# Kernel tuning notes

Measured on AMD Instinct MI355X. Metric: run time of the kernel, lower is better.

The kernel has to match this reference:

```python
import jax, jax.numpy as jnp
import numpy as np

HIDDEN = 256
HEADS = 8
HEAD_DIM = HIDDEN // HEADS
N = 4096
EPS = 1e-5


def setup_inputs() -> dict:
    key = jax.random.key(0)
    ks = jax.random.split(key, 16)
    s = HIDDEN ** -0.5
    inp = {
        "A": jax.random.uniform(ks[0], (N, N), dtype=jnp.float32),
        "h": jax.random.normal(ks[1], (N, HIDDEN), dtype=jnp.float32),
        # Linear layers stored torch-style as [out, in]
        "Wq": jax.random.normal(ks[2], (HIDDEN, HIDDEN), jnp.float32) * s,
        "bq": jnp.zeros((HIDDEN,), jnp.float32),
        "Wk": jax.random.normal(ks[3], (HIDDEN, HIDDEN), jnp.float32) * s,
        "bk": jnp.zeros((HIDDEN,), jnp.float32),
        "Wv": jax.random.normal(ks[4], (HIDDEN, HIDDEN), jnp.float32) * s,
        "bv": jnp.zeros((HIDDEN,), jnp.float32),
        "Wo": jax.random.normal(ks[5], (HIDDEN, HIDDEN), jnp.float32) * s,
        "bo": jnp.zeros((HIDDEN,), jnp.float32),
        "W1": jax.random.normal(ks[6], (2 * HIDDEN, HIDDEN), jnp.float32) * s,
        "c1": jnp.zeros((2 * HIDDEN,), jnp.float32),
        "W2": jax.random.normal(ks[7], (HIDDEN, 2 * HIDDEN), jnp.float32) * (2 * HIDDEN) ** -0.5,
        "c2": jnp.zeros((HIDDEN,), jnp.float32),
        "g1": jnp.ones((HIDDEN,), jnp.float32),
        "be1": jnp.zeros((HIDDEN,), jnp.float32),
        "g2": jnp.ones((HIDDEN,), jnp.float32),
        "be2": jnp.zeros((HIDDEN,), jnp.float32),
    }
    return inp


def _batchnorm(x, gamma, beta):
    # BatchNorm1d training mode: biased batch stats over node axis
    mean = x.mean(axis=0)
    var = ((x - mean) ** 2).mean(axis=0)
    return (x - mean) * jax.lax.rsqrt(var + EPS) * gamma + beta


def _mha(A, h, Wq, bq, Wk, bk, Wv, bv, Wo, bo):
    n = h.shape[0]
    scaling = HEAD_DIM ** -0.5
    # NOTE: raw reshape [N, H*d] -> (H, N, d), exactly as the torch code (no transpose)
    q = ((h @ Wq.T + bq).reshape(HEADS, n, HEAD_DIM)) * scaling
    k = (h @ Wk.T + bk).reshape(HEADS, n, HEAD_DIM)
    v = (h @ Wv.T + bv).reshape(HEADS, n, HEAD_DIM)
    t = jnp.einsum('hnd,hmd->hnm', q, k)          # [H, N, N]
    attn = jax.nn.softmax(t * A, axis=2)          # multiplicative adjacency mask
    out = jnp.einsum('hnm,hmd->hnd', attn, v)     # [H, N, d]
    return out.reshape(n, -1) @ Wo.T + bo         # raw reshape back, as in torch


def reference(A, h, Wq, bq, Wk, bk, Wv, bv, Wo, bo, W1, c1, W2, c2, g1, be1, g2, be2):
    h1 = h
    x = _mha(A, h, Wq, bq, Wk, bk, Wv, bv, Wo, bo)
    x = _batchnorm(x + h1, g1, be1)
    h2 = x
    x = jax.nn.relu(x @ W1.T + c1) @ W2.T + c2
    return _batchnorm(h2 + x, g2, be2)
```

## Files before the change

kernel.cpp:

```cpp
#include <hip/hip_runtime.h>

#define N_NODES 4096
#define HID 256
#define NHEADS 8
#define HDIM 32
#define EPSV 1e-5f
#define M2LOG 11.541560327111707f

typedef __bf16 bf16x8 __attribute__((ext_vector_type(8)));
typedef __bf16 bf16x4 __attribute__((ext_vector_type(4)));
typedef float f32x4 __attribute__((ext_vector_type(4)));

__device__ inline float fexp2(float x) {
    float r;
    asm("v_exp_f32 %0, %1" : "=v"(r) : "v"(x));
    return r;
}

__device__ inline uint4 pack8(float4 a, float4 b) {
    bf16x8 p;
    p[0]=(__bf16)a.x; p[1]=(__bf16)a.y; p[2]=(__bf16)a.z; p[3]=(__bf16)a.w;
    p[4]=(__bf16)b.x; p[5]=(__bf16)b.y; p[6]=(__bf16)b.z; p[7]=(__bf16)b.w;
    return __builtin_bit_cast(uint4, p);
}
__device__ inline float4 nmad4(float4 x, float4 s, float4 sh) {
    return make_float4(fmaf(x.x,s.x,sh.x), fmaf(x.y,s.y,sh.y),
                       fmaf(x.z,s.z,sh.z), fmaf(x.w,s.w,sh.w));
}

__launch_bounds__(256)
__global__ void gemm_mfma(const float* __restrict__ X, const float* __restrict__ W,
                          const float* __restrict__ bias, const float* __restrict__ resid,
                          float* __restrict__ C,
                          const float* __restrict__ nscale, const float* __restrict__ nshift,
                          const float* __restrict__ rscale, const float* __restrict__ rshift,
                          float* __restrict__ psum, float* __restrict__ pq,
                          int M, int N, int K, float scale, int do_relu) {
    __shared__ uint4 xl[2][512];
    __shared__ uint4 wl[2][512];
    const int bm = blockIdx.x * 64, bn = blockIdx.y * 64;
    const int t = threadIdx.x;
    const int w = t >> 6, l = t & 63, g = l >> 4, nl = l & 15;
    const int srow = t >> 3, seg = t & 7;
    const int sx = (seg & 3) << 1;
    const int d0 = seg*64 + (srow ^ sx);
    const int d1 = seg*64 + ((srow + 32) ^ sx);
    const float* xp = X + (size_t)(bm + srow)*K + seg*8;
    const float* wp = W + (size_t)(bn + srow)*K + seg*8;
    const size_t rstep = (size_t)32*K;

    f32x4 acc[4];
    #pragma unroll
    for (int nf = 0; nf < 4; ++nf) acc[nf] = (f32x4){0.f,0.f,0.f,0.f};

    {
        float4 x0 = *(const float4*)(xp),          x1 = *(const float4*)(xp + 4);
        float4 x2 = *(const float4*)(xp + rstep),  x3 = *(const float4*)(xp + rstep + 4);
        if (nscale) {
            float4 s0 = *(const float4*)(nscale + seg*8), s1 = *(const float4*)(nscale + seg*8 + 4);
            float4 h0 = *(const float4*)(nshift + seg*8), h1 = *(const float4*)(nshift + seg*8 + 4);
            x0 = nmad4(x0,s0,h0); x1 = nmad4(x1,s1,h1);
            x2 = nmad4(x2,s0,h0); x3 = nmad4(x3,s1,h1);
        }
        float4 w0 = *(const float4*)(wp),          w1 = *(const float4*)(wp + 4);
        float4 w2 = *(const float4*)(wp + rstep),  w3 = *(const float4*)(wp + rstep + 4);
        xl[0][d0] = pack8(x0, x1); xl[0][d1] = pack8(x2, x3);
        wl[0][d0] = pack8(w0, w1); wl[0][d1] = pack8(w2, w3);
    }
    __syncthreads();

    for (int k0 = 0; k0 < K; k0 += 64) {
        const int cur = (k0 >> 6) & 1;
        const bool nxt = (k0 + 64) < K;
        float4 nx0, nx1, nx2, nx3, nw0, nw1, nw2, nw3;
        if (nxt) {
            const int kk = k0 + 64;
            nx0 = *(const float4*)(xp + kk);          nx1 = *(const float4*)(xp + kk + 4);
            nx2 = *(const float4*)(xp + rstep + kk);  nx3 = *(const float4*)(xp + rstep + kk + 4);
            if (nscale) {
                float4 s0 = *(const float4*)(nscale + kk + seg*8), s1 = *(const float4*)(nscale + kk + seg*8 + 4);
                float4 h0 = *(const float4*)(nshift + kk + seg*8), h1 = *(const float4*)(nshift + kk + seg*8 + 4);
                nx0 = nmad4(nx0,s0,h0); nx1 = nmad4(nx1,s1,h1);
                nx2 = nmad4(nx2,s0,h0); nx3 = nmad4(nx3,s1,h1);
            }
            nw0 = *(const float4*)(wp + kk);          nw1 = *(const float4*)(wp + kk + 4);
            nw2 = *(const float4*)(wp + rstep + kk);  nw3 = *(const float4*)(wp + rstep + kk + 4);
        }
        __builtin_amdgcn_s_setprio(1);
        #pragma unroll
        for (int ks = 0; ks < 2; ++ks) {
            bf16x8 af = __builtin_bit_cast(bf16x8, xl[cur][(ks*4 + g)*64 + ((w*16 + nl) ^ (g << 1))]);
            #pragma unroll
            for (int nf = 0; nf < 4; ++nf) {
                bf16x8 bfr = __builtin_bit_cast(bf16x8, wl[cur][(ks*4 + g)*64 + ((nf*16 + nl) ^ (g << 1))]);
                acc[nf] = __builtin_amdgcn_mfma_f32_16x16x32_bf16(af, bfr, acc[nf], 0, 0, 0);
            }
        }
        __builtin_amdgcn_s_setprio(0);
        if (nxt) {
            xl[cur^1][d0] = pack8(nx0, nx1); xl[cur^1][d1] = pack8(nx2, nx3);
            wl[cur^1][d0] = pack8(nw0, nw1); wl[cur^1][d1] = pack8(nw2, nw3);
        }
        __syncthreads();
    }

    float colS[4] = {0.f,0.f,0.f,0.f}, colQ[4] = {0.f,0.f,0.f,0.f};
    #pragma unroll
    for (int nf = 0; nf < 4; ++nf) {
        const int col = bn + nf*16 + nl;
        const float bb = bias[col];
        float rs = 1.f, rh = 0.f;
        if (rscale) { rs = rscale[col]; rh = rshift[col]; }
        #pragma unroll
        for (int r = 0; r < 4; ++r) {
            const int row = bm + w*16 + g*4 + r;
            float v = acc[nf][r] + bb;
            if (resid) {
                float rv = resid[(size_t)row*N + col];
                v += rscale ? fmaf(rv, rs, rh) : rv;
            }
            v *= scale;
            if (do_relu) v = fmaxf(v, 0.f);
            C[(size_t)row*N + col] = v;
            colS[nf] += v;
            colQ[nf] = fmaf(v, v, colQ[nf]);
        }
    }
    if (psum) {
        float* cs = (float*)&xl[0][0];
        float* cq = cs + 1024;
        #pragma unroll
        for (int nf = 0; nf < 4; ++nf) {
            const int idx = (w*4 + g)*64 + nf*16 + nl;
            cs[idx] = colS[nf];
            cq[idx] = colQ[nf];
        }
        __syncthreads();
        if (t < 64) {
            float s = 0.f, q = 0.f;
            #pragma unroll
            for (int i = 0; i < 16; ++i) { s += cs[i*64 + t]; q += cq[i*64 + t]; }
            psum[blockIdx.x*HID + bn + t] = s;
            pq[blockIdx.x*HID + bn + t]   = q;
        }
    }
}

__launch_bounds__(256)
__global__ void gemm_wo(const float* __restrict__ Opart, const float* __restrict__ Lpart,
                        int nsplit, const float* __restrict__ W,
                        const float* __restrict__ bias, const float* __restrict__ resid,
                        float* __restrict__ C, float* __restrict__ psum, float* __restrict__ pq) {
    const int N = 256, K = 256;
    __shared__ uint4 xl[2][512];
    __shared__ uint4 wl[2][512];
    const int bm = blockIdx.x * 64, bn = blockIdx.y * 64;
    const int t = threadIdx.x;
    const int w = t >> 6, l = t & 63, g = l >> 4, nl = l & 15;
    const int srow = t >> 3, seg = t & 7;
    const int sx = (seg & 3) << 1;
    const int d0 = seg*64 + (srow ^ sx);
    const int d1 = seg*64 + ((srow + 32) ^ sx);
    const float* wp = W + (size_t)(bn + srow)*K + seg*8;
    const size_t rstep = (size_t)32*K;

    auto cl = [&](int row, int kk, float4& a, float4& b) {
        const size_t flat = (size_t)row*256 + kk;
        const int hn = (int)(flat >> 5);
        float L = 0.f;
        a = make_float4(0.f,0.f,0.f,0.f);
        b = make_float4(0.f,0.f,0.f,0.f);
        for (int z = 0; z < nsplit; ++z) {
            L += Lpart[z*32768 + hn];
            float4 u = *(const float4*)(Opart + (size_t)z*1048576 + flat);
            float4 v = *(const float4*)(Opart + (size_t)z*1048576 + flat + 4);
            a.x += u.x; a.y += u.y; a.z += u.z; a.w += u.w;
            b.x += v.x; b.y += v.y; b.z += v.z; b.w += v.w;
        }
        const float inv = 1.f / L;
        a.x *= inv; a.y *= inv; a.z *= inv; a.w *= inv;
        b.x *= inv; b.y *= inv; b.z *= inv; b.w *= inv;
    };

    f32x4 acc[4];
    #pragma unroll
    for (int nf = 0; nf < 4; ++nf) acc[nf] = (f32x4){0.f,0.f,0.f,0.f};

    {
        float4 x0, x1, x2, x3;
        cl(bm + srow,      seg*8, x0, x1);
        cl(bm + srow + 32, seg*8, x2, x3);
        float4 w0 = *(const float4*)(wp),          w1 = *(const float4*)(wp + 4);
        float4 w2 = *(const float4*)(wp + rstep),  w3 = *(const float4*)(wp + rstep + 4);
        xl[0][d0] = pack8(x0, x1); xl[0][d1] = pack8(x2, x3);
        wl[0][d0] = pack8(w0, w1); wl[0][d1] = pack8(w2, w3);
    }
    __syncthreads();

    for (int k0 = 0; k0 < K; k0 += 64) {
        const int cur = (k0 >> 6) & 1;
        const bool nxt = (k0 + 64) < K;
        float4 nx0, nx1, nx2, nx3, nw0, nw1, nw2, nw3;
        if (nxt) {
            const int kk = k0 + 64 + seg*8;
            cl(bm + srow,      kk, nx0, nx1);
            cl(bm + srow + 32, kk, nx2, nx3);
            nw0 = *(const float4*)(wp + k0 + 64);          nw1 = *(const float4*)(wp + k0 + 68);
            nw2 = *(const float4*)(wp + rstep + k0 + 64);  nw3 = *(const float4*)(wp + rstep + k0 + 68);
        }
        __builtin_amdgcn_s_setprio(1);
        #pragma unroll
        for (int ks = 0; ks < 2; ++ks) {
            bf16x8 af = __builtin_bit_cast(bf16x8, xl[cur][(ks*4 + g)*64 + ((w*16 + nl) ^ (g << 1))]);
            #pragma unroll
            for (int nf = 0; nf < 4; ++nf) {
                bf16x8 bfr = __builtin_bit_cast(bf16x8, wl[cur][(ks*4 + g)*64 + ((nf*16 + nl) ^ (g << 1))]);
                acc[nf] = __builtin_amdgcn_mfma_f32_16x16x32_bf16(af, bfr, acc[nf], 0, 0, 0);
            }
        }
        __builtin_amdgcn_s_setprio(0);
        if (nxt) {
            xl[cur^1][d0] = pack8(nx0, nx1); xl[cur^1][d1] = pack8(nx2, nx3);
            wl[cur^1][d0] = pack8(nw0, nw1); wl[cur^1][d1] = pack8(nw2, nw3);
        }
        __syncthreads();
    }

    float colS[4] = {0.f,0.f,0.f,0.f}, colQ[4] = {0.f,0.f,0.f,0.f};
    #pragma unroll
    for (int nf = 0; nf < 4; ++nf) {
        const int col = bn + nf*16 + nl;
        const float bb = bias[col];
        #pragma unroll
        for (int r = 0; r < 4; ++r) {
            const int row = bm + w*16 + g*4 + r;
            float v = acc[nf][r] + bb + resid[(size_t)row*N + col];
            C[(size_t)row*N + col] = v;
            colS[nf] += v;
            colQ[nf] = fmaf(v, v, colQ[nf]);
        }
    }
    {
        float* cs = (float*)&xl[0][0];
        float* cq = cs + 1024;
        #pragma unroll
        for (int nf = 0; nf < 4; ++nf) {
            const int idx = (w*4 + g)*64 + nf*16 + nl;
            cs[idx] = colS[nf];
            cq[idx] = colQ[nf];
        }
        __syncthreads();
        if (t < 64) {
            float s = 0.f, q = 0.f;
            #pragma unroll
            for (int i = 0; i < 16; ++i) { s += cs[i*64 + t]; q += cq[i*64 + t]; }
            psum[blockIdx.x*HID + bn + t] = s;
            pq[blockIdx.x*HID + bn + t]   = q;
        }
    }
}

__launch_bounds__(256)
__global__ void gemm_qkv(const float* __restrict__ X,
                         const float* __restrict__ Wq, const float* __restrict__ Wk,
                         const float* __restrict__ Wv, const float* __restrict__ bq,
                         const float* __restrict__ bk, const float* __restrict__ bv,
                         __bf16* __restrict__ qhat, __bf16* __restrict__ khat,
                         __bf16* __restrict__ vhat) {
    const int K = 256;
    __shared__ uint4 xl[2][512];
    __shared__ uint4 wl[2][512];
    const int z = blockIdx.z;
    const float* W = (z == 0) ? Wq : (z == 1) ? Wk : Wv;
    const float* bias = (z == 0) ? bq : (z == 1) ? bk : bv;
    __bf16* hat = (z == 0) ? qhat : (z == 1) ? khat : vhat;
    const float scale = (z == 0) ? 0.25506595325f : 1.f;

    const int bm = blockIdx.x * 64, bn = blockIdx.y * 64;
    const int t = threadIdx.x;
    const int w = t >> 6, l = t & 63, g = l >> 4, nl = l & 15;
    const int srow = t >> 3, seg = t & 7;
    const int sx = (seg & 3) << 1;
    const int d0 = seg*64 + (srow ^ sx);
    const int d1 = seg*64 + ((srow + 32) ^ sx);
    const float* xp = X + (size_t)(bm + srow)*K + seg*8;
    const float* wp = W + (size_t)(bn + srow)*K + seg*8;
    const size_t rstep = (size_t)32*K;

    f32x4 acc[4];
    #pragma unroll
    for (int nf = 0; nf < 4; ++nf) acc[nf] = (f32x4){0.f,0.f,0.f,0.f};

    {
        float4 x0 = *(const float4*)(xp),          x1 = *(const float4*)(xp + 4);
        float4 x2 = *(const float4*)(xp + rstep),  x3 = *(const float4*)(xp + rstep + 4);
        float4 w0 = *(const float4*)(wp),          w1 = *(const float4*)(wp + 4);
        float4 w2 = *(const float4*)(wp + rstep),  w3 = *(const float4*)(wp + rstep + 4);
        xl[0][d0] = pack8(x0, x1); xl[0][d1] = pack8(x2, x3);
        wl[0][d0] = pack8(w0, w1); wl[0][d1] = pack8(w2, w3);
    }
    __syncthreads();

    for (int k0 = 0; k0 < K; k0 += 64) {
        const int cur = (k0 >> 6) & 1;
        const bool nxt = (k0 + 64) < K;
        float4 nx0, nx1, nx2, nx3, nw0, nw1, nw2, nw3;
        if (nxt) {
            nx0 = *(const float4*)(xp + k0 + 64);          nx1 = *(const float4*)(xp + k0 + 68);
            nx2 = *(const float4*)(xp + rstep + k0 + 64);  nx3 = *(const float4*)(xp + rstep + k0 + 68);
            nw0 = *(const float4*)(wp + k0 + 64);          nw1 = *(const float4*)(wp + k0 + 68);
            nw2 = *(const float4*)(wp + rstep + k0 + 64);  nw3 = *(const float4*)(wp + rstep + k0 + 68);
        }
        __builtin_amdgcn_s_setprio(1);
        #pragma unroll
        for (int ks = 0; ks < 2; ++ks) {
            bf16x8 af = __builtin_bit_cast(bf16x8, xl[cur][(ks*4 + g)*64 + ((w*16 + nl) ^ (g << 1))]);
            #pragma unroll
            for (int nf = 0; nf < 4; ++nf) {
                bf16x8 bfr = __builtin_bit_cast(bf16x8, wl[cur][(ks*4 + g)*64 + ((nf*16 + nl) ^ (g << 1))]);
                acc[nf] = __builtin_amdgcn_mfma_f32_16x16x32_bf16(af, bfr, acc[nf], 0, 0, 0);
            }
        }
        __builtin_amdgcn_s_setprio(0);
        if (nxt) {
            xl[cur^1][d0] = pack8(nx0, nx1); xl[cur^1][d1] = pack8(nx2, nx3);
            wl[cur^1][d0] = pack8(nw0, nw1); wl[cur^1][d1] = pack8(nw2, nw3);
        }
        __syncthreads();
    }

    #pragma unroll
    for (int nf = 0; nf < 4; ++nf) {
        const int col = bn + nf*16 + nl;
        const float bb = bias[col];
        #pragma unroll
        for (int r = 0; r < 4; ++r) {
            const int row = bm + w*16 + g*4 + r;
            float v = (acc[nf][r] + bb) * scale;
            const int hh = row >> 9;
            const int nn = ((row & 511) << 3) | (col >> 5);
            hat[((size_t)(hh*4096 + nn))*32 + (col & 31)] = (__bf16)v;
        }
    }
}

__launch_bounds__(256)
__global__ void transpose_vhat(const __bf16* __restrict__ vhat, __bf16* __restrict__ vT) {
    const int h = blockIdx.y, n0 = blockIdx.x * 64;
    __shared__ __bf16 tile[64][40];
    const int t = threadIdx.x;
    {
        int n = t >> 2, dd0 = (t & 3) * 8;
        *(uint4*)&tile[n][dd0] = *(const uint4*)(vhat + ((size_t)(h*4096 + n0 + n))*32 + dd0);
    }
    __syncthreads();
    {
        int d = t >> 3, ns = (t & 7) * 8;
        uint4 ov;
        __bf16* op = (__bf16*)&ov;
        #pragma unroll
        for (int j = 0; j < 8; ++j) op[j] = tile[ns + j][d];
        *(uint4*)(vT + ((size_t)(h*32 + d))*4096 + n0 + ns) = ov;
    }
}

__launch_bounds__(512, 2)
__global__ void attn_mfma(const __bf16* __restrict__ qh_, const __bf16* __restrict__ kh,
                          const __bf16* __restrict__ vT, const float* __restrict__ A,
                          float* __restrict__ Opart, float* __restrict__ Lpart, int mlen) {
    __shared__ float A_lds[2][64][68];
    __shared__ uint4 p_lds[8][4][64];

    const int t = threadIdx.x;
    const int w = t >> 6, l = t & 63;
    const int g = l >> 4, nl = l & 15;
    const int n0 = blockIdx.x * 64;
    const int z = blockIdx.y;
    const int m_begin = z * mlen;
    const int nsteps = mlen >> 6;

    bf16x8 qf[4];
    #pragma unroll
    for (int nf = 0; nf < 4; ++nf)
        qf[nf] = *(const bf16x8*)(qh_ + ((size_t)(w*4096 + n0 + nf*16 + nl))*32 + g*8);

    f32x4 oacc[4][2];
    #pragma unroll
    for (int nf = 0; nf < 4; ++nf) {
        oacc[nf][0] = (f32x4){0.f,0.f,0.f,0.f};
        oacc[nf][1] = (f32x4){0.f,0.f,0.f,0.f};
    }
    float Li[4] = {0.f, 0.f, 0.f, 0.f};

    const int aq = t >> 3, am = (t & 7) * 8;
    const float* Abase = A + (size_t)(n0 + aq)*N_NODES + m_begin + am;
    const __bf16* kbase = kh + ((size_t)w*4096 + nl)*32 + g*8;
    const __bf16* vbase = vT + ((size_t)w*32 + nl)*4096 + g*8;

    *(float4*)&A_lds[0][aq][am]   = *(const float4*)(Abase);
    *(float4*)&A_lds[0][aq][am+4] = *(const float4*)(Abase + 4);
    __syncthreads();

    for (int s = 0; s < nsteps; ++s) {
        const int cur = s & 1;
        const int m0 = m_begin + s*64;
        const bool nxt = (s + 1) < nsteps;
        float4 a0n, a1n;
        if (nxt) {
            a0n = *(const float4*)(Abase + (s+1)*64);
            a1n = *(const float4*)(Abase + (s+1)*64 + 4);
        }
        bf16x8 kf[4], vf[4];
        #pragma unroll
        for (int tt = 0; tt < 4; ++tt)
            kf[tt] = *(const bf16x8*)(kbase + (size_t)(m0 + tt*16)*32);
        #pragma unroll
        for (int half = 0; half < 2; ++half)
            #pragma unroll
            for (int dt = 0; dt < 2; ++dt)
                vf[half*2+dt] = *(const bf16x8*)(vbase + (size_t)dt*16*4096 + m0 + half*32);
        __builtin_amdgcn_sched_barrier(0);

        #pragma unroll
        for (int half = 0; half < 2; ++half) {
            #pragma unroll
            for (int tt2 = 0; tt2 < 2; ++tt2) {
                const int tt = half*2 + tt2;
                f32x4 st[4];
                __builtin_amdgcn_s_setprio(1);
                #pragma unroll
                for (int nf = 0; nf < 4; ++nf) {
                    f32x4 zz = (f32x4){0.f,0.f,0.f,0.f};
                    st[nf] = __builtin_amdgcn_mfma_f32_16x16x32_bf16(kf[tt], qf[nf], zz, 0, 0, 0);
                }
                __builtin_amdgcn_s_setprio(0);
                #pragma unroll
                for (int nf = 0; nf < 4; ++nf) {
                    const f32x4 a4 = *(const f32x4*)&A_lds[cur][nf*16 + nl][tt*16 + g*4];
                    float p0 = fexp2(fmaf(st[nf][0], a4[0], -M2LOG));
                    float p1 = fexp2(fmaf(st[nf][1], a4[1], -M2LOG));
                    float p2 = fexp2(fmaf(st[nf][2], a4[2], -M2LOG));
                    float p3 = fexp2(fmaf(st[nf][3], a4[3], -M2LOG));
                    Li[nf] += (p0 + p1) + (p2 + p3);
                    bf16x4 pk;
                    pk[0] = (__bf16)p0; pk[1] = (__bf16)p1;
                    pk[2] = (__bf16)p2; pk[3] = (__bf16)p3;
                    const int gm = tt2*2 + (g >> 1);
                    *(bf16x4*)((char*)&p_lds[w][nf][0] + (gm*16 + (nl ^ (gm << 1)))*16 + (g & 1)*8) = pk;
                }
            }
            __builtin_amdgcn_s_setprio(1);
            #pragma unroll
            for (int nf = 0; nf < 4; ++nf) {
                bf16x8 pf = __builtin_bit_cast(bf16x8, p_lds[w][nf][g*16 + (nl ^ (g << 1))]);
                oacc[nf][0] = __builtin_amdgcn_mfma_f32_16x16x32_bf16(vf[half*2+0], pf, oacc[nf][0], 0, 0, 0);
                oacc[nf][1] = __builtin_amdgcn_mfma_f32_16x16x32_bf16(vf[half*2+1], pf, oacc[nf][1], 0, 0, 0);
            }
            __builtin_amdgcn_s_setprio(0);
        }

        if (nxt) {
            *(float4*)&A_lds[cur^1][aq][am]   = a0n;
            *(float4*)&A_lds[cur^1][aq][am+4] = a1n;
        }
        __syncthreads();
    }

    #pragma unroll
    for (int nf = 0; nf < 4; ++nf) {
        Li[nf] += __shfl_xor(Li[nf], 16);
        Li[nf] += __shfl_xor(Li[nf], 32);
        const int nq = n0 + nf*16 + nl;
        float* ob = Opart + ((size_t)(z*NHEADS + w)*4096 + nq)*32;
        *(float4*)(ob + 0*16 + g*4) = make_float4(oacc[nf][0][0], oacc[nf][0][1],
                                                  oacc[nf][0][2], oacc[nf][0][3]);
        *(float4*)(ob + 1*16 + g*4) = make_float4(oacc[nf][1][0], oacc[nf][1][1],
                                                  oacc[nf][1][2], oacc[nf][1][3]);
        if (g == 0)
            Lpart[(z*NHEADS + w)*4096 + nq] = Li[nf];
    }
}

__launch_bounds__(256)
__global__ void colstats_fin(const float* __restrict__ ps, const float* __restrict__ pq,
                             const float* __restrict__ gam, const float* __restrict__ bet,
                             float* __restrict__ scl, float* __restrict__ shf) {
    const int c = threadIdx.x;
    float s = 0.f, q = 0.f;
    #pragma unroll 8
    for (int b = 0; b < 64; ++b) { s += ps[b*HID + c]; q += pq[b*HID + c]; }
    const float m = s * (1.f/4096.f);
    const float rstd = rsqrtf(q*(1.f/4096.f) - m*m + EPSV);
    const float sc = rstd * gam[c];
    scl[c] = sc;
    shf[c] = fmaf(-m, sc, bet[c]);
}

__launch_bounds__(256)
__global__ void bnorm_apply4(const float* __restrict__ X, const float* __restrict__ scl,
                             const float* __restrict__ shf, float* __restrict__ Y) {
    const int base = (blockIdx.x * 256 + threadIdx.x) * 4;
    const int c = base & (HID - 1);
    float4 x = *(const float4*)(X + base);
    float4 o;
    o.x = fmaf(x.x, scl[c+0], shf[c+0]);
    o.y = fmaf(x.y, scl[c+1], shf[c+1]);
    o.z = fmaf(x.z, scl[c+2], shf[c+2]);
    o.w = fmaf(x.w, scl[c+3], shf[c+3]);
    *(float4*)(Y + base) = o;
}

extern "C" void kernel_launch(void* const* d_in, const int* in_sizes, int n_in,
                              void* d_out, int out_size, void* d_ws, size_t ws_size,
                              hipStream_t stream) {
    const float* A  = (const float*)d_in[0];
    const float* h  = (const float*)d_in[1];
    const float* Wq = (const float*)d_in[2];
    const float* bq = (const float*)d_in[3];
    const float* Wk = (const float*)d_in[4];
    const float* bk = (const float*)d_in[5];
    const float* Wv = (const float*)d_in[6];
    const float* bv = (const float*)d_in[7];
    const float* Wo = (const float*)d_in[8];
    const float* bo = (const float*)d_in[9];
    const float* W1 = (const float*)d_in[10];
    const float* c1 = (const float*)d_in[11];
    const float* W2 = (const float*)d_in[12];
    const float* c2 = (const float*)d_in[13];
    const float* g1 = (const float*)d_in[14];
    const float* be1= (const float*)d_in[15];
    const float* g2 = (const float*)d_in[16];
    const float* be2= (const float*)d_in[17];

    char* wsb = (char*)d_ws;
    const size_t MiB = (size_t)1 << 20;
    const int nsplit = (ws_size >= 43*MiB) ? 8 : (ws_size >= 26*MiB) ? 4 : 2;
    const int mlen = N_NODES / nsplit;

    __bf16* qhat = (__bf16*)(wsb + 0*MiB);
    __bf16* khat = (__bf16*)(wsb + 2*MiB);
    __bf16* vhat = (__bf16*)(wsb + 4*MiB);
    __bf16* vT   = (__bf16*)(wsb + 6*MiB);
    float* Opart = (float*)(wsb + 8*MiB);
    float* Lpart = (float*)(wsb + 8*MiB + (size_t)nsplit*4*MiB);
    char* statb  = wsb + 8*MiB + (size_t)nsplit*4*MiB + 1*MiB;
    float* partS = (float*)statb;
    float* partQ = partS + 64*HID;
    float* scale1 = partQ + 64*HID;
    float* shift1 = scale1 + HID;
    float* scale2 = shift1 + HID;
    float* shift2 = scale2 + HID;
    float* Y1 = (float*)(wsb + 4*MiB);
    float* F1 = (float*)(wsb + 8*MiB);
    float* Y2 = (float*)(wsb + 0*MiB);

    gemm_qkv<<<dim3(64, 4, 3), 256, 0, stream>>>(h, Wq, Wk, Wv, bq, bk, bv, qhat, khat, vhat);
    transpose_vhat<<<dim3(64, 8), 256, 0, stream>>>(vhat, vT);

    attn_mfma<<<dim3(64, nsplit), 512, 0, stream>>>(qhat, khat, vT, A, Opart, Lpart, mlen);

    gemm_wo<<<dim3(64, 4), 256, 0, stream>>>(Opart, Lpart, nsplit, Wo, bo, h, Y1, partS, partQ);
    colstats_fin<<<1, 256, 0, stream>>>(partS, partQ, g1, be1, scale1, shift1);

    gemm_mfma<<<dim3(64, 8), 256, 0, stream>>>(Y1, W1, c1, nullptr, F1,
                                               scale1, shift1, nullptr, nullptr,
                                               nullptr, nullptr, 4096, 512, 256, 1.f, 1);
    gemm_mfma<<<dim3(64, 4), 256, 0, stream>>>(F1, W2, c2, Y1, Y2,
                                               nullptr, nullptr, scale1, shift1,
                                               partS, partQ, 4096, 256, 512, 1.f, 0);
    colstats_fin<<<1, 256, 0, stream>>>(partS, partQ, g2, be2, scale2, shift2);
    bnorm_apply4<<<1024, 256, 0, stream>>>(Y2, scale2, shift2, (float*)d_out);
}
```

Before: 130.2 us.

## Fuse batchnorm stat finalization into consumers and halve attention query tile

The two single-block colstats_fin launches are removed. Each consuming kernel (both FFN GEMMs and a merged finalize-and-apply kernel) now recomputes per-channel scale and shift from the partial sums into shared memory. This drops launches and serialization points at the cost of redundant reduction work per block. Separately, the attention kernel processes 32 query rows per block instead of 64, doubling the grid and raising the occupancy hint to 6 blocks per CU. That gives more parallelism but reuses each K/V fragment across fewer queries.

```diff
diff --git a/kernel.cpp b/kernel.cpp
--- a/kernel.cpp
+++ b/kernel.cpp
@@ -32,12 +32,15 @@
 __global__ void gemm_mfma(const float* __restrict__ X, const float* __restrict__ W,
                           const float* __restrict__ bias, const float* __restrict__ resid,
                           float* __restrict__ C,
-                          const float* __restrict__ nscale, const float* __restrict__ nshift,
-                          const float* __restrict__ rscale, const float* __restrict__ rshift,
+                          const float* __restrict__ pSin, const float* __restrict__ pQin,
+                          const float* __restrict__ gamin, const float* __restrict__ betin,
+                          int norm_x, int norm_r,
                           float* __restrict__ psum, float* __restrict__ pq,
                           int M, int N, int K, float scale, int do_relu) {
     __shared__ uint4 xl[2][512];
     __shared__ uint4 wl[2][512];
+    __shared__ __align__(16) float nsc[256];
+    __shared__ __align__(16) float nsh[256];
     const int bm = blockIdx.x * 64, bn = blockIdx.y * 64;
     const int t = threadIdx.x;
     const int w = t >> 6, l = t & 63, g = l >> 4, nl = l & 15;
@@ -49,6 +52,18 @@
     const float* wp = W + (size_t)(bn + srow)*K + seg*8;
     const size_t rstep = (size_t)32*K;
 
+    if (pSin) {
+        float s = 0.f, q = 0.f;
+        #pragma unroll 8
+        for (int b = 0; b < 64; ++b) { s += pSin[b*HID + t]; q += pQin[b*HID + t]; }
+        const float m = s * (1.f/4096.f);
+        const float rstd = rsqrtf(q*(1.f/4096.f) - m*m + EPSV);
+        const float sc = rstd * gamin[t];
+        nsc[t] = sc;
+        nsh[t] = fmaf(-m, sc, betin[t]);
+        __syncthreads();
+    }
+
     f32x4 acc[4];
     #pragma unroll
     for (int nf = 0; nf < 4; ++nf) acc[nf] = (f32x4){0.f,0.f,0.f,0.f};
@@ -56,9 +71,9 @@
     {
         float4 x0 = *(const float4*)(xp),          x1 = *(const float4*)(xp + 4);
         float4 x2 = *(const float4*)(xp + rstep),  x3 = *(const float4*)(xp + rstep + 4);
-        if (nscale) {
-            float4 s0 = *(const float4*)(nscale + seg*8), s1 = *(const float4*)(nscale + seg*8 + 4);
-            float4 h0 = *(const float4*)(nshift + seg*8), h1 = *(const float4*)(nshift + seg*8 + 4);
+        if (norm_x) {
+            float4 s0 = *(const float4*)(nsc + seg*8), s1 = *(const float4*)(nsc + seg*8 + 4);
+            float4 h0 = *(const float4*)(nsh + seg*8), h1 = *(const float4*)(nsh + seg*8 + 4);
             x0 = nmad4(x0,s0,h0); x1 = nmad4(x1,s1,h1);
             x2 = nmad4(x2,s0,h0); x3 = nmad4(x3,s1,h1);
         }
@@ -77,9 +92,9 @@
             const int kk = k0 + 64;
             nx0 = *(const float4*)(xp + kk);          nx1 = *(const float4*)(xp + kk + 4);
             nx2 = *(const float4*)(xp + rstep + kk);  nx3 = *(const float4*)(xp + rstep + kk + 4);
-            if (nscale) {
-                float4 s0 = *(const float4*)(nscale + kk + seg*8), s1 = *(const float4*)(nscale + kk + seg*8 + 4);
-                float4 h0 = *(const float4*)(nshift + kk + seg*8), h1 = *(const float4*)(nshift + kk + seg*8 + 4);
+            if (norm_x) {
+                float4 s0 = *(const float4*)(nsc + kk + seg*8), s1 = *(const float4*)(nsc + kk + seg*8 + 4);
+                float4 h0 = *(const float4*)(nsh + kk + seg*8), h1 = *(const float4*)(nsh + kk + seg*8 + 4);
                 nx0 = nmad4(nx0,s0,h0); nx1 = nmad4(nx1,s1,h1);
                 nx2 = nmad4(nx2,s0,h0); nx3 = nmad4(nx3,s1,h1);
             }
@@ -110,14 +125,14 @@
         const int col = bn + nf*16 + nl;
         const float bb = bias[col];
         float rs = 1.f, rh = 0.f;
-        if (rscale) { rs = rscale[col]; rh = rshift[col]; }
+        if (norm_r) { rs = nsc[col]; rh = nsh[col]; }
         #pragma unroll
         for (int r = 0; r < 4; ++r) {
             const int row = bm + w*16 + g*4 + r;
             float v = acc[nf][r] + bb;
             if (resid) {
                 float rv = resid[(size_t)row*N + col];
-                v += rscale ? fmaf(rv, rs, rh) : rv;
+                v += norm_r ? fmaf(rv, rs, rh) : rv;
             }
             v *= scale;
             if (do_relu) v = fmaxf(v, 0.f);
@@ -364,52 +379,49 @@
     }
 }
 
-__launch_bounds__(512, 2)
+__launch_bounds__(512, 6)
 __global__ void attn_mfma(const __bf16* __restrict__ qh_, const __bf16* __restrict__ kh,
                           const __bf16* __restrict__ vT, const float* __restrict__ A,
                           float* __restrict__ Opart, float* __restrict__ Lpart, int mlen) {
-    __shared__ float A_lds[2][64][68];
-    __shared__ uint4 p_lds[8][4][64];
+    __shared__ float A_lds[2][32][68];
+    __shared__ uint4 p_lds[8][2][64];
 
     const int t = threadIdx.x;
     const int w = t >> 6, l = t & 63;
     const int g = l >> 4, nl = l & 15;
-    const int n0 = blockIdx.x * 64;
+    const int n0 = blockIdx.x * 32;
     const int z = blockIdx.y;
     const int m_begin = z * mlen;
     const int nsteps = mlen >> 6;
 
-    bf16x8 qf[4];
-    #pragma unroll
-    for (int nf = 0; nf < 4; ++nf)
+    bf16x8 qf[2];
+    #pragma unroll
+    for (int nf = 0; nf < 2; ++nf)
         qf[nf] = *(const bf16x8*)(qh_ + ((size_t)(w*4096 + n0 + nf*16 + nl))*32 + g*8);
 
-    f32x4 oacc[4][2];
-    #pragma unroll
-    for (int nf = 0; nf < 4; ++nf) {
+    f32x4 oacc[2][2];
+    #pragma unroll
+    for (int nf = 0; nf < 2; ++nf) {
         oacc[nf][0] = (f32x4){0.f,0.f,0.f,0.f};
         oacc[nf][1] = (f32x4){0.f,0.f,0.f,0.f};
     }
-    float Li[4] = {0.f, 0.f, 0.f, 0.f};
-
-    const int aq = t >> 3, am = (t & 7) * 8;
+    float Li[2] = {0.f, 0.f};
+
+    const int aq = t >> 4, am = (t & 15) * 4;
     const float* Abase = A + (size_t)(n0 + aq)*N_NODES + m_begin + am;
     const __bf16* kbase = kh + ((size_t)w*4096 + nl)*32 + g*8;
     const __bf16* vbase = vT + ((size_t)w*32 + nl)*4096 + g*8;
 
-    *(float4*)&A_lds[0][aq][am]   = *(const float4*)(Abase);
-    *(float4*)&A_lds[0][aq][am+4] = *(const float4*)(Abase + 4);
+    *(float4*)&A_lds[0][aq][am] = *(const float4*)(Abase);
     __syncthreads();
 
     for (int s = 0; s < nsteps; ++s) {
         const int cur = s & 1;
         const int m0 = m_begin + s*64;
         const bool nxt = (s + 1) < nsteps;
-        float4 a0n, a1n;
-        if (nxt) {
-            a0n = *(const float4*)(Abase + (s+1)*64);
-            a1n = *(const float4*)(Abase + (s+1)*64 + 4);
-        }
+        float4 an;
+        if (nxt) an = *(const float4*)(Abase + (s+1)*64);
+
         bf16x8 kf[4], vf[4];
         #pragma unroll
         for (int tt = 0; tt < 4; ++tt)
@@ -426,16 +438,16 @@
             #pragma unroll
             for (int tt2 = 0; tt2 < 2; ++tt2) {
                 const int tt = half*2 + tt2;
-                f32x4 st[4];
+                f32x4 st[2];
                 __builtin_amdgcn_s_setprio(1);
                 #pragma unroll
-                for (int nf = 0; nf < 4; ++nf) {
+                for (int nf = 0; nf < 2; ++nf) {
                     f32x4 zz = (f32x4){0.f,0.f,0.f,0.f};
                     st[nf] = __builtin_amdgcn_mfma_f32_16x16x32_bf16(kf[tt], qf[nf], zz, 0, 0, 0);
                 }
                 __builtin_amdgcn_s_setprio(0);
                 #pragma unroll
-                for (int nf = 0; nf < 4; ++nf) {
+                for (int nf = 0; nf < 2; ++nf) {
                     const f32x4 a4 = *(const f32x4*)&A_lds[cur][nf*16 + nl][tt*16 + g*4];
                     float p0 = fexp2(fmaf(st[nf][0], a4[0], -M2LOG));
                     float p1 = fexp2(fmaf(st[nf][1], a4[1], -M2LOG));
@@ -451,7 +463,7 @@
             }
             __builtin_amdgcn_s_setprio(1);
             #pragma unroll
-            for (int nf = 0; nf < 4; ++nf) {
+            for (int nf = 0; nf < 2; ++nf) {
                 bf16x8 pf = __builtin_bit_cast(bf16x8, p_lds[w][nf][g*16 + (nl ^ (g << 1))]);
                 oacc[nf][0] = __builtin_amdgcn_mfma_f32_16x16x32_bf16(vf[half*2+0], pf, oacc[nf][0], 0, 0, 0);
                 oacc[nf][1] = __builtin_amdgcn_mfma_f32_16x16x32_bf16(vf[half*2+1], pf, oacc[nf][1], 0, 0, 0);
@@ -460,14 +472,13 @@
         }
 
         if (nxt) {
-            *(float4*)&A_lds[cur^1][aq][am]   = a0n;
-            *(float4*)&A_lds[cur^1][aq][am+4] = a1n;
-        }
-        __syncthreads();
-    }
-
-    #pragma unroll
-    for (int nf = 0; nf < 4; ++nf) {
+            *(float4*)&A_lds[cur^1][aq][am] = an;
+        }
+        __syncthreads();
+    }
+
+    #pragma unroll
+    for (int nf = 0; nf < 2; ++nf) {
         Li[nf] += __shfl_xor(Li[nf], 16);
         Li[nf] += __shfl_xor(Li[nf], 32);
         const int nq = n0 + nf*16 + nl;
@@ -482,32 +493,37 @@
 }
 
 __launch_bounds__(256)
-__global__ void colstats_fin(const float* __restrict__ ps, const float* __restrict__ pq,
-                             const float* __restrict__ gam, const float* __restrict__ bet,
-                             float* __restrict__ scl, float* __restrict__ shf) {
-    const int c = threadIdx.x;
-    float s = 0.f, q = 0.f;
-    #pragma unroll 8
-    for (int b = 0; b < 64; ++b) { s += ps[b*HID + c]; q += pq[b*HID + c]; }
-    const float m = s * (1.f/4096.f);
-    const float rstd = rsqrtf(q*(1.f/4096.f) - m*m + EPSV);
-    const float sc = rstd * gam[c];
-    scl[c] = sc;
-    shf[c] = fmaf(-m, sc, bet[c]);
-}
-
-__launch_bounds__(256)
-__global__ void bnorm_apply4(const float* __restrict__ X, const float* __restrict__ scl,
-                             const float* __restrict__ shf, float* __restrict__ Y) {
-    const int base = (blockIdx.x * 256 + threadIdx.x) * 4;
-    const int c = base & (HID - 1);
-    float4 x = *(const float4*)(X + base);
-    float4 o;
-    o.x = fmaf(x.x, scl[c+0], shf[c+0]);
-    o.y = fmaf(x.y, scl[c+1], shf[c+1]);
-    o.z = fmaf(x.z, scl[c+2], shf[c+2]);
-    o.w = fmaf(x.w, scl[c+3], shf[c+3]);
-    *(float4*)(Y + base) = o;
+__global__ void bnorm_fin_apply(const float* __restrict__ X,
+                                const float* __restrict__ pS, const float* __restrict__ pQ,
+                                const float* __restrict__ gam, const float* __restrict__ bet,
+                                float* __restrict__ Y) {
+    __shared__ __align__(16) float sc[256];
+    __shared__ __align__(16) float sh[256];
+    const int t = threadIdx.x;
+    {
+        float s = 0.f, q = 0.f;
+        #pragma unroll 8
+        for (int b = 0; b < 64; ++b) { s += pS[b*HID + t]; q += pQ[b*HID + t]; }
+        const float m = s * (1.f/4096.f);
+        const float rstd = rsqrtf(q*(1.f/4096.f) - m*m + EPSV);
+        const float scv = rstd * gam[t];
+        sc[t] = scv;
+        sh[t] = fmaf(-m, scv, bet[t]);
+    }
+    __syncthreads();
+    const int base0 = (blockIdx.x * 256 + t) * 16;
+    #pragma unroll
+    for (int j = 0; j < 4; ++j) {
+        const int base = base0 + j*4;
+        const int c = base & (HID - 1);
+        float4 x = *(const float4*)(X + base);
+        float4 o;
+        o.x = fmaf(x.x, sc[c+0], sh[c+0]);
+        o.y = fmaf(x.y, sc[c+1], sh[c+1]);
+        o.z = fmaf(x.z, sc[c+2], sh[c+2]);
+        o.w = fmaf(x.w, sc[c+3], sh[c+3]);
+        *(float4*)(Y + base) = o;
+    }
 }
 
 extern "C" void kernel_launch(void* const* d_in, const int* in_sizes, int n_in,
@@ -544,12 +560,10 @@
     float* Opart = (float*)(wsb + 8*MiB);
     float* Lpart = (float*)(wsb + 8*MiB + (size_t)nsplit*4*MiB);
     char* statb  = wsb + 8*MiB + (size_t)nsplit*4*MiB + 1*MiB;
-    float* partS = (float*)statb;
-    float* partQ = partS + 64*HID;
-    float* scale1 = partQ + 64*HID;
-    float* shift1 = scale1 + HID;
-    float* scale2 = shift1 + HID;
-    float* shift2 = scale2 + HID;
+    float* partS1 = (float*)statb;
+    float* partQ1 = partS1 + 64*HID;
+    float* partS2 = partQ1 + 64*HID;
+    float* partQ2 = partS2 + 64*HID;
     float* Y1 = (float*)(wsb + 4*MiB);
     float* F1 = (float*)(wsb + 8*MiB);
     float* Y2 = (float*)(wsb + 0*MiB);
@@ -557,17 +571,16 @@
     gemm_qkv<<<dim3(64, 4, 3), 256, 0, stream>>>(h, Wq, Wk, Wv, bq, bk, bv, qhat, khat, vhat);
     transpose_vhat<<<dim3(64, 8), 256, 0, stream>>>(vhat, vT);
 
-    attn_mfma<<<dim3(64, nsplit), 512, 0, stream>>>(qhat, khat, vT, A, Opart, Lpart, mlen);
-
-    gemm_wo<<<dim3(64, 4), 256, 0, stream>>>(Opart, Lpart, nsplit, Wo, bo, h, Y1, partS, partQ);
-    colstats_fin<<<1, 256, 0, stream>>>(partS, partQ, g1, be1, scale1, shift1);
+    attn_mfma<<<dim3(128, nsplit), 512, 0, stream>>>(qhat, khat, vT, A, Opart, Lpart, mlen);
+
+    gemm_wo<<<dim3(64, 4), 256, 0, stream>>>(Opart, Lpart, nsplit, Wo, bo, h, Y1, partS1, partQ1);
 
     gemm_mfma<<<dim3(64, 8), 256, 0, stream>>>(Y1, W1, c1, nullptr, F1,
-                                               scale1, shift1, nullptr, nullptr,
+                                               partS1, partQ1, g1, be1, 1, 0,
                                                nullptr, nullptr, 4096, 512, 256, 1.f, 1);
     gemm_mfma<<<dim3(64, 4), 256, 0, stream>>>(F1, W2, c2, Y1, Y2,
-                                               nullptr, nullptr, scale1, shift1,
-                                               partS, partQ, 4096, 256, 512, 1.f, 0);
-    colstats_fin<<<1, 256, 0, stream>>>(partS, partQ, g2, be2, scale2, shift2);
-    bnorm_apply4<<<1024, 256, 0, stream>>>(Y2, scale2, shift2, (float*)d_out);
-}
+                                               partS1, partQ1, g1, be1, 0, 1,
+                                               partS2, partQ2, 4096, 256, 512, 1.f, 0);
+
+    bnorm_fin_apply<<<256, 256, 0, stream>>>(Y2, partS2, partQ2, g2, be2, (float*)d_out);
+}
```

Result: slower. 197.5 us (+51.7%).
